# Performance work log

Measured on AMD Instinct MI355X. Metric: run time of the kernel, lower is better.

## Reference

```python
import jax, jax.numpy as jnp
import numpy as np

N_NODES = 50000   # rows of x / output of NF-spmm
M_NODES = 50000   # output of FN-spmm
N_EDGES = 800000
NFEAT, N_HIDDEN, NCLASS = 300, 256, 20
N_IDX = 5000


def setup_inputs() -> dict:
    key = jax.random.key(0)
    ks = jax.random.split(key, 12)
    x = jax.random.normal(ks[0], (N_NODES, NFEAT), dtype=jnp.float32)
    fn_rows = jax.random.randint(ks[1], (N_EDGES,), 0, M_NODES)
    fn_cols = jax.random.randint(ks[2], (N_EDGES,), 0, N_NODES)
    fn_vals = jax.random.uniform(ks[3], (N_EDGES,), dtype=jnp.float32)
    nf_rows = jax.random.randint(ks[4], (N_EDGES,), 0, N_NODES)
    nf_cols = jax.random.randint(ks[5], (N_EDGES,), 0, M_NODES)
    nf_vals = jax.random.uniform(ks[6], (N_EDGES,), dtype=jnp.float32)
    idx = jax.random.randint(ks[7], (N_IDX,), 0, N_NODES)
    # learned parameters (pygcn-style GraphConvolution: spmm(adj, x @ W) + b)
    W1 = jax.random.normal(ks[8], (NFEAT, N_HIDDEN), dtype=jnp.float32) / np.sqrt(NFEAT)
    b1 = jnp.zeros((N_HIDDEN,), dtype=jnp.float32)
    W2 = jax.random.normal(ks[9], (N_HIDDEN, NCLASS), dtype=jnp.float32) / np.sqrt(N_HIDDEN)
    b2 = jnp.zeros((NCLASS,), dtype=jnp.float32)
    return {"x": x, "fn_rows": fn_rows, "fn_cols": fn_cols, "fn_vals": fn_vals,
            "nf_rows": nf_rows, "nf_cols": nf_cols, "nf_vals": nf_vals,
            "idx": idx, "W1": W1, "b1": b1, "W2": W2, "b2": b2}


def _spmm(rows, cols, vals, dense, n_out):
    # sparse(COO) @ dense: gather source rows, scale by edge value, scatter-add.
    return jax.ops.segment_sum(vals[:, None] * dense[cols], rows, num_segments=n_out)


def reference(x, fn_rows, fn_cols, fn_vals, nf_rows, nf_cols, nf_vals, idx, W1, b1, W2, b2):
    # gc1: FN @ (x @ W1) + b1, then relu  (dropout is identity in eval mode)
    h = jax.nn.relu(_spmm(fn_rows, fn_cols, fn_vals, x @ W1, M_NODES) + b1)
    # gc2: NF @ (h @ W2) + b2
    logits = _spmm(nf_rows, nf_cols, nf_vals, h @ W2, N_NODES) + b2
    return jax.nn.softmax(logits, axis=1)[idx]
```

## Files before the change

kernel.cpp:

```cpp
#include <hip/hip_runtime.h>

#define N_NODES 50000
#define M_NODES 50000
#define N_EDGES 800000
#define NFEAT   300
#define NHID    256
#define NCLASS  20
#define N_IDX   5000
#define KTILES  10
#define NTOT    (M_NODES + N_NODES)
#define MARKW   ((N_NODES + 31) / 32)
#define GEMM1_BLOCKS ((N_NODES + 63) / 64)
#define EB4_BLOCKS   ((N_EDGES + 1023) / 1024)

typedef __attribute__((ext_vector_type(8))) short bf16x8;
typedef __attribute__((ext_vector_type(4))) float f32x4;

__device__ inline unsigned short f2bf(float f) {
    unsigned u = __float_as_uint(f);
    u += 0x7fff + ((u >> 16) & 1);
    return (unsigned short)(u >> 16);
}
__device__ inline float bf2f(unsigned short h) { return __uint_as_float((unsigned)h << 16); }
__device__ inline float bflo(unsigned v) { return __uint_as_float(v << 16); }
__device__ inline float bfhi(unsigned v) { return __uint_as_float(v & 0xffff0000u); }

__global__ __launch_bounds__(256) void prep_w1_mark_kernel(const float* __restrict__ W1,
                                                           unsigned short* __restrict__ w1h,
                                                           unsigned short* __restrict__ w1l,
                                                           const int* __restrict__ idx,
                                                           unsigned* __restrict__ markbits) {
    if (blockIdx.x < 320) {
        int id = blockIdx.x * 256 + threadIdx.x;
        int col = id & 255;
        int k   = id >> 8;
        float v = (k < NFEAT) ? W1[(size_t)k * NHID + col] : 0.f;
        unsigned short hi = f2bf(v);
        unsigned short lo = f2bf(v - bf2f(hi));
        size_t off = (size_t)(k >> 5) * (256 * 32) + (size_t)col * 32 + (k & 31);
        w1h[off] = hi;
        w1l[off] = lo;
    } else {
        int i = (blockIdx.x - 320) * 256 + threadIdx.x;
        if (i < N_IDX) {
            int r = idx[i];
            atomicOr(&markbits[r >> 5], 1u << (r & 31));
        }
    }
}

__global__ __launch_bounds__(256) void hist_both_kernel(const int* __restrict__ fn_rows,
                                                        const int* __restrict__ nf_rows,
                                                        const unsigned* __restrict__ markbits,
                                                        int* __restrict__ counts,
                                                        unsigned short* __restrict__ fn_rank,
                                                        unsigned short* __restrict__ nf_rank) {
    const int base = blockIdx.x * 1024 + threadIdx.x;
    int r[4], r2[4], m2[4];
#pragma unroll
    for (int k = 0; k < 4; ++k) {
        int e = base + k * 256;
        r[k]  = (e < N_EDGES) ? fn_rows[e] : -1;
        r2[k] = (e < N_EDGES) ? nf_rows[e] : -1;
    }
#pragma unroll
    for (int k = 0; k < 4; ++k)
        m2[k] = (r2[k] >= 0) ? (int)((markbits[r2[k] >> 5] >> (r2[k] & 31)) & 1u) : 0;
#pragma unroll
    for (int k = 0; k < 4; ++k) {
        if (r[k] >= 0) {
            int p = atomicAdd(&counts[r[k]], 1);
            fn_rank[base + k * 256] = (unsigned short)p;
        }
    }
#pragma unroll
    for (int k = 0; k < 4; ++k) {
        if (m2[k]) {
            int p = atomicAdd(&counts[M_NODES + r2[k]], 1);
            nf_rank[base + k * 256] = (unsigned short)p;
        }
    }
}

__global__ __launch_bounds__(256) void scan_chunk_kernel(const int* __restrict__ counts,
                                                         int* __restrict__ chunk_incl,
                                                         int* __restrict__ chunk_sums, int n) {
    __shared__ int lds[256];
    int i = blockIdx.x * 256 + threadIdx.x;
    int v = (i < n) ? counts[i] : 0;
    lds[threadIdx.x] = v;
    __syncthreads();
    for (int off = 1; off < 256; off <<= 1) {
        int t = (threadIdx.x >= off) ? lds[threadIdx.x - off] : 0;
        __syncthreads();
        lds[threadIdx.x] += t;
        __syncthreads();
    }
    if (i < n) chunk_incl[i] = lds[threadIdx.x];
    if (threadIdx.x == 255) chunk_sums[blockIdx.x] = lds[255];
}

__global__ __launch_bounds__(512) void scan_sums_kernel(const int* __restrict__ chunk_sums,
                                                        int* __restrict__ chunk_off,
                                                        int* __restrict__ row_ptr_end, int nchunks) {
    __shared__ int lds[512];
    int tid = threadIdx.x;
    int v = (tid < nchunks) ? chunk_sums[tid] : 0;
    lds[tid] = v;
    __syncthreads();
    for (int off = 1; off < 512; off <<= 1) {
        int t = (tid >= off) ? lds[tid - off] : 0;
        __syncthreads();
        lds[tid] += t;
        __syncthreads();
    }
    if (tid < nchunks) chunk_off[tid] = lds[tid] - v;
    if (tid == nchunks - 1) *row_ptr_end = lds[tid];
}

__global__ void scan_apply_kernel(const int* __restrict__ counts,
                                  const int* __restrict__ chunk_incl,
                                  const int* __restrict__ chunk_off,
                                  int* __restrict__ row_ptr, int n) {
    int i = blockIdx.x * 256 + threadIdx.x;
    if (i < n) row_ptr[i] = chunk_incl[i] - counts[i] + chunk_off[blockIdx.x];
}

__global__ __launch_bounds__(256) void gemm1_scatter_kernel(
        const float* __restrict__ x,
        const unsigned short* __restrict__ w1h,
        const unsigned short* __restrict__ w1l,
        unsigned short* __restrict__ xwb,
        const int* __restrict__ fn_rows, const int* __restrict__ fn_cols,
        const float* __restrict__ fn_vals,
        const int* __restrict__ nf_rows, const int* __restrict__ nf_cols,
        const float* __restrict__ nf_vals,
        const unsigned* __restrict__ markbits,
        const int* __restrict__ row_ptr,
        const unsigned short* __restrict__ fn_rank,
        const unsigned short* __restrict__ nf_rank,
        uint2* __restrict__ csr_cv) {
    __shared__ unsigned short Ah[2][64 * 40];
    __shared__ unsigned short Al[2][64 * 40];

    if (blockIdx.x >= GEMM1_BLOCKS) {
        const int base = (blockIdx.x - GEMM1_BLOCKS) * 1024 + threadIdx.x;
#pragma unroll
        for (int k = 0; k < 4; ++k) {
            int e = base + k * 256;
            if (e < N_EDGES) {
                int r = fn_rows[e];
                int p = row_ptr[r] + fn_rank[e];
                csr_cv[p] = make_uint2((unsigned)fn_cols[e], __float_as_uint(fn_vals[e]));
            }
        }
#pragma unroll
        for (int k = 0; k < 4; ++k) {
            int e = base + k * 256;
            if (e < N_EDGES) {
                int r2 = nf_rows[e];
                if ((markbits[r2 >> 5] >> (r2 & 31)) & 1u) {
                    int p = row_ptr[M_NODES + r2] + nf_rank[e];
                    csr_cv[p] = make_uint2((unsigned)nf_cols[e], __float_as_uint(nf_vals[e]));
                }
            }
        }
        return;
    }

    const int tid  = threadIdx.x;
    const int lane = tid & 63;
    const int wv   = tid >> 6;
    const int l15  = lane & 15;
    const int g    = lane >> 4;
    const int row0 = blockIdx.x * 64;

    const int sr = tid >> 2;
    const int sc = tid & 3;
    const bool rowok = (row0 + sr) < N_NODES;
    const float* __restrict__ xrow = x + (size_t)(row0 + sr) * NFEAT;

    float cur[8], nxt[8];
    if (rowok) {
        float4 v0 = *(const float4*)&xrow[sc * 8 + 0];
        float4 v1 = *(const float4*)&xrow[sc * 8 + 4];
        cur[0] = v0.x; cur[1] = v0.y; cur[2] = v0.z; cur[3] = v0.w;
        cur[4] = v1.x; cur[5] = v1.y; cur[6] = v1.z; cur[7] = v1.w;
    } else {
#pragma unroll
        for (int j = 0; j < 8; ++j) cur[j] = 0.f;
    }

    f32x4 acc[4][4];
#pragma unroll
    for (int mf = 0; mf < 4; ++mf)
#pragma unroll
        for (int nf = 0; nf < 4; ++nf) acc[mf][nf] = (f32x4){0.f, 0.f, 0.f, 0.f};

    for (int t = 0; t < KTILES; ++t) {
        if (t < KTILES - 1) {
            const int k0 = (t + 1) * 32 + sc * 8;
            if (t + 1 < KTILES - 1) {
                if (rowok) {
                    float4 v0 = *(const float4*)&xrow[k0 + 0];
                    float4 v1 = *(const float4*)&xrow[k0 + 4];
                    nxt[0] = v0.x; nxt[1] = v0.y; nxt[2] = v0.z; nxt[3] = v0.w;
                    nxt[4] = v1.x; nxt[5] = v1.y; nxt[6] = v1.z; nxt[7] = v1.w;
                } else {
#pragma unroll
                    for (int j = 0; j < 8; ++j) nxt[j] = 0.f;
                }
            } else {
#pragma unroll
                for (int j = 0; j < 8; ++j) {
                    int k = k0 + j;
                    nxt[j] = (rowok && k < NFEAT) ? xrow[k] : 0.f;
                }
            }
        }

        {
            bf16x8 hv, lv;
#pragma unroll
            for (int j = 0; j < 8; ++j) {
                unsigned short h = f2bf(cur[j]);
                hv[j] = (short)h;
                lv[j] = (short)f2bf(cur[j] - bf2f(h));
            }
            const int wo = sr * 40 + sc * 8;
            *(bf16x8*)&Ah[t & 1][wo] = hv;
            *(bf16x8*)&Al[t & 1][wo] = lv;
        }
        __syncthreads();

        const int b = t & 1;
        bf16x8 ah[4], al[4];
#pragma unroll
        for (int mf = 0; mf < 4; ++mf) {
            const int ao = (mf * 16 + l15) * 40 + g * 8;
            ah[mf] = *(const bf16x8*)&Ah[b][ao];
            al[mf] = *(const bf16x8*)&Al[b][ao];
        }
        bf16x8 bh[4], bl[4];
#pragma unroll
        for (int nf = 0; nf < 4; ++nf) {
            const size_t bo = (size_t)t * 8192 + (size_t)(wv * 64 + nf * 16 + l15) * 32 + g * 8;
            bh[nf] = *(const bf16x8*)&w1h[bo];
            bl[nf] = *(const bf16x8*)&w1l[bo];
        }
#pragma unroll
        for (int mf = 0; mf < 4; ++mf)
#pragma unroll
            for (int nf = 0; nf < 4; ++nf) {
                acc[mf][nf] = __builtin_amdgcn_mfma_f32_16x16x32_bf16(ah[mf], bh[nf], acc[mf][nf], 0, 0, 0);
                acc[mf][nf] = __builtin_amdgcn_mfma_f32_16x16x32_bf16(ah[mf], bl[nf], acc[mf][nf], 0, 0, 0);
                acc[mf][nf] = __builtin_amdgcn_mfma_f32_16x16x32_bf16(al[mf], bh[nf], acc[mf][nf], 0, 0, 0);
            }
#pragma unroll
        for (int j = 0; j < 8; ++j) cur[j] = nxt[j];
    }

    const int colb = wv * 64;
#pragma unroll
    for (int mf = 0; mf < 4; ++mf) {
        const int rg0 = row0 + mf * 16 + g * 4;
#pragma unroll
        for (int nf = 0; nf < 4; ++nf) {
            const int cg = colb + nf * 16 + l15;
#pragma unroll
            for (int j = 0; j < 4; ++j) {
                const int rg = rg0 + j;
                if (rg < N_NODES) xwb[(size_t)rg * NHID + cg] = f2bf(acc[mf][nf][j]);
            }
        }
    }
}

__global__ __launch_bounds__(128) void spmm_fn_kernel(const int* __restrict__ row_ptr,
                                                      const uint2* __restrict__ csr_cv,
                                                      const unsigned* __restrict__ xwb,
                                                      const float* __restrict__ b1,
                                                      unsigned* __restrict__ hb) {
    const int r = blockIdx.x;
    const int t = threadIdx.x;
    const int s = row_ptr[r], e = row_ptr[r + 1];
    float a0 = 0.f, a1 = 0.f;
    int j = s;
    for (; j + 3 < e; j += 4) {
        uint2 cv0 = csr_cv[j],     cv1 = csr_cv[j + 1];
        uint2 cv2 = csr_cv[j + 2], cv3 = csr_cv[j + 3];
        float v0 = __uint_as_float(cv0.y), v1 = __uint_as_float(cv1.y);
        float v2 = __uint_as_float(cv2.y), v3 = __uint_as_float(cv3.y);
        unsigned x0 = xwb[(size_t)cv0.x * 128 + t];
        unsigned x1 = xwb[(size_t)cv1.x * 128 + t];
        unsigned x2 = xwb[(size_t)cv2.x * 128 + t];
        unsigned x3 = xwb[(size_t)cv3.x * 128 + t];
        a0 += v0 * bflo(x0); a1 += v0 * bfhi(x0);
        a0 += v1 * bflo(x1); a1 += v1 * bfhi(x1);
        a0 += v2 * bflo(x2); a1 += v2 * bfhi(x2);
        a0 += v3 * bflo(x3); a1 += v3 * bfhi(x3);
    }
    for (; j < e; ++j) {
        uint2 cv = csr_cv[j];
        float v = __uint_as_float(cv.y);
        unsigned xv = xwb[(size_t)cv.x * 128 + t];
        a0 += v * bflo(xv); a1 += v * bfhi(xv);
    }
    float2 bv = *(const float2*)&b1[t * 2];
    float o0 = fmaxf(a0 + bv.x, 0.f);
    float o1 = fmaxf(a1 + bv.y, 0.f);
    hb[(size_t)r * 128 + t] = ((unsigned)f2bf(o1) << 16) | (unsigned)f2bf(o0);
}

__global__ __launch_bounds__(256) void gemm2_kernel(const uint4* __restrict__ hb,
                                                    const float* __restrict__ W2,
                                                    float* __restrict__ hw) {
    __shared__ float w2s[NHID * NCLASS];
    for (int i = threadIdx.x; i < NHID * NCLASS; i += 256) w2s[i] = W2[i];
    __syncthreads();
    int gid = blockIdx.x * 256 + threadIdx.x;
    if (gid >= N_NODES * NCLASS) return;
    int row = gid / NCLASS;
    int col = gid - row * NCLASS;
    const uint4* hp = &hb[(size_t)row * 32];
    float acc = 0.f;
#pragma unroll 4
    for (int k8 = 0; k8 < 32; ++k8) {
        uint4 hv = hp[k8];
        int k = k8 * 8;
        acc += bflo(hv.x) * w2s[(k + 0) * NCLASS + col];
        acc += bfhi(hv.x) * w2s[(k + 1) * NCLASS + col];
        acc += bflo(hv.y) * w2s[(k + 2) * NCLASS + col];
        acc += bfhi(hv.y) * w2s[(k + 3) * NCLASS + col];
        acc += bflo(hv.z) * w2s[(k + 4) * NCLASS + col];
        acc += bfhi(hv.z) * w2s[(k + 5) * NCLASS + col];
        acc += bflo(hv.w) * w2s[(k + 6) * NCLASS + col];
        acc += bfhi(hv.w) * w2s[(k + 7) * NCLASS + col];
    }
    hw[gid] = acc;
}

__global__ __launch_bounds__(64) void spmm_nf_softmax_kernel(const int* __restrict__ idx,
                                                             const int* __restrict__ row_ptr,
                                                             const uint2* __restrict__ csr_cv,
                                                             const float* __restrict__ hw,
                                                             const float* __restrict__ b2,
                                                             float* __restrict__ out) {
    const int b    = blockIdx.x;
    const int lane = threadIdx.x;
    const int r = idx[b];
    const int s = row_ptr[M_NODES + r], e = row_ptr[M_NODES + r + 1];

    float acc[NCLASS];
#pragma unroll
    for (int k = 0; k < NCLASS; ++k) acc[k] = 0.f;

    for (int j = s + lane; j < e; j += 64) {
        uint2 cv = csr_cv[j];
        int   c = (int)cv.x;
        float v = __uint_as_float(cv.y);
        const float4* hp = (const float4*)&hw[(size_t)c * NCLASS];
        float4 h0 = hp[0], h1 = hp[1], h2 = hp[2], h3 = hp[3], h4 = hp[4];
        acc[0]  += v * h0.x; acc[1]  += v * h0.y; acc[2]  += v * h0.z; acc[3]  += v * h0.w;
        acc[4]  += v * h1.x; acc[5]  += v * h1.y; acc[6]  += v * h1.z; acc[7]  += v * h1.w;
        acc[8]  += v * h2.x; acc[9]  += v * h2.y; acc[10] += v * h2.z; acc[11] += v * h2.w;
        acc[12] += v * h3.x; acc[13] += v * h3.y; acc[14] += v * h3.z; acc[15] += v * h3.w;
        acc[16] += v * h4.x; acc[17] += v * h4.y; acc[18] += v * h4.z; acc[19] += v * h4.w;
    }

#pragma unroll
    for (int k = 0; k < NCLASS; ++k) {
#pragma unroll
        for (int off = 1; off < 64; off <<= 1) acc[k] += __shfl_xor(acc[k], off, 64);
    }

    if (lane == 0) {
        float v[NCLASS];
        float m = -1e30f;
#pragma unroll
        for (int k = 0; k < NCLASS; ++k) {
            v[k] = acc[k] + b2[k];
            m = fmaxf(m, v[k]);
        }
        float sum = 0.f;
#pragma unroll
        for (int k = 0; k < NCLASS; ++k) {
            v[k] = __expf(v[k] - m);
            sum += v[k];
        }
        float inv = 1.f / sum;
#pragma unroll
        for (int k = 0; k < NCLASS; ++k) out[(size_t)b * NCLASS + k] = v[k] * inv;
    }
}

extern "C" void kernel_launch(void* const* d_in, const int* in_sizes, int n_in,
                              void* d_out, int out_size, void* d_ws, size_t ws_size,
                              hipStream_t stream) {
    const float* x       = (const float*)d_in[0];
    const int*   fn_rows = (const int*)  d_in[1];
    const int*   fn_cols = (const int*)  d_in[2];
    const float* fn_vals = (const float*)d_in[3];
    const int*   nf_rows = (const int*)  d_in[4];
    const int*   nf_cols = (const int*)  d_in[5];
    const float* nf_vals = (const float*)d_in[6];
    const int*   idx     = (const int*)  d_in[7];
    const float* W1      = (const float*)d_in[8];
    const float* b1      = (const float*)d_in[9];
    const float* W2      = (const float*)d_in[10];
    const float* b2      = (const float*)d_in[11];
    float* out = (float*)d_out;

    size_t off = 0;
    auto alloc = [&](size_t bytes) {
        void* p = (char*)d_ws + off;
        off += (bytes + 255) & ~(size_t)255;
        return p;
    };
    unsigned short* xwb = (unsigned short*)alloc((size_t)N_NODES * NHID * 2);
    unsigned*       hb  = (unsigned*)      alloc((size_t)M_NODES * NHID * 2);
    float* hw       = (float*)alloc((size_t)M_NODES * NCLASS * 4);
    int*      counts   = (int*)     alloc((size_t)NTOT * 4);
    unsigned* markbits = (unsigned*)alloc((size_t)MARKW * 4);
    int*   row_ptr  = (int*)  alloc((size_t)(NTOT + 1) * 4);
    uint2* csr_cv   = (uint2*)alloc((size_t)2 * N_EDGES * 8);
    unsigned short* fn_rank = (unsigned short*)alloc((size_t)N_EDGES * 2);
    unsigned short* nf_rank = (unsigned short*)alloc((size_t)N_EDGES * 2);
    int*   chunk_incl = (int*)alloc((size_t)NTOT * 4);
    int*   chunk_sums = (int*)alloc(512 * 4);
    int*   chunk_off  = (int*)alloc(512 * 4);
    unsigned short* w1h = (unsigned short*)alloc((size_t)KTILES * 256 * 32 * 2);
    unsigned short* w1l = (unsigned short*)alloc((size_t)KTILES * 256 * 32 * 2);
    (void)ws_size; (void)n_in; (void)in_sizes; (void)out_size;

    const int NCHUNKS_ALL = (NTOT + 255) / 256;

    size_t zlen = (size_t)((char*)markbits - (char*)counts) + (size_t)MARKW * 4;
    hipMemsetAsync(counts, 0, zlen, stream);

    prep_w1_mark_kernel<<<320 + (N_IDX + 255) / 256, 256, 0, stream>>>(W1, w1h, w1l, idx, markbits);

    hist_both_kernel<<<EB4_BLOCKS, 256, 0, stream>>>(fn_rows, nf_rows, markbits, counts, fn_rank, nf_rank);
    scan_chunk_kernel<<<NCHUNKS_ALL, 256, 0, stream>>>(counts, chunk_incl, chunk_sums, NTOT);
    scan_sums_kernel<<<1, 512, 0, stream>>>(chunk_sums, chunk_off, &row_ptr[NTOT], NCHUNKS_ALL);
    scan_apply_kernel<<<NCHUNKS_ALL, 256, 0, stream>>>(counts, chunk_incl, chunk_off, row_ptr, NTOT);

    gemm1_scatter_kernel<<<GEMM1_BLOCKS + EB4_BLOCKS, 256, 0, stream>>>(
        x, w1h, w1l, xwb,
        fn_rows, fn_cols, fn_vals, nf_rows, nf_cols, nf_vals,
        markbits, row_ptr, fn_rank, nf_rank, csr_cv);

    spmm_fn_kernel<<<M_NODES, 128, 0, stream>>>(row_ptr, csr_cv, (const unsigned*)xwb, b1, hb);

    gemm2_kernel<<<(N_NODES * NCLASS + 255) / 256, 256, 0, stream>>>((const uint4*)hb, W2, hw);

    spmm_nf_softmax_kernel<<<N_IDX, 64, 0, stream>>>(idx, row_ptr, csr_cv, hw, b2, out);
}
```

Before: 201.8 us.

## Use MFMA for second GEMM and merge scan offset kernels

Replaces the scalar LDS-based h@W2 kernel with an MFMA bf16 kernel that uses hi/lo split W2 tiles prepared in the prep kernel, padding NCLASS to 32 columns. It also fuses the single-block chunk-sum scan and the apply kernel into one kernel, where each block reduces its preceding chunk sums itself. This removes a kernel launch and the scalar FMA work in gemm2, at the cost of redundant prefix reductions per block and extra prep work for W2.

```diff
diff --git a/kernel.cpp b/kernel.cpp
--- a/kernel.cpp
+++ b/kernel.cpp
@@ -8,6 +8,7 @@
 #define NCLASS  20
 #define N_IDX   5000
 #define KTILES  10
+#define K2TILES 8
 #define NTOT    (M_NODES + N_NODES)
 #define MARKW   ((N_NODES + 31) / 32)
 #define GEMM1_BLOCKS ((N_NODES + 63) / 64)
@@ -25,11 +26,14 @@
 __device__ inline float bflo(unsigned v) { return __uint_as_float(v << 16); }
 __device__ inline float bfhi(unsigned v) { return __uint_as_float(v & 0xffff0000u); }
 
-__global__ __launch_bounds__(256) void prep_w1_mark_kernel(const float* __restrict__ W1,
-                                                           unsigned short* __restrict__ w1h,
-                                                           unsigned short* __restrict__ w1l,
-                                                           const int* __restrict__ idx,
-                                                           unsigned* __restrict__ markbits) {
+__global__ __launch_bounds__(256) void prep_kernel(const float* __restrict__ W1,
+                                                   unsigned short* __restrict__ w1h,
+                                                   unsigned short* __restrict__ w1l,
+                                                   const int* __restrict__ idx,
+                                                   unsigned* __restrict__ markbits,
+                                                   const float* __restrict__ W2,
+                                                   unsigned short* __restrict__ w2h,
+                                                   unsigned short* __restrict__ w2l) {
     if (blockIdx.x < 320) {
         int id = blockIdx.x * 256 + threadIdx.x;
         int col = id & 255;
@@ -40,12 +44,22 @@
         size_t off = (size_t)(k >> 5) * (256 * 32) + (size_t)col * 32 + (k & 31);
         w1h[off] = hi;
         w1l[off] = lo;
-    } else {
+    } else if (blockIdx.x < 340) {
         int i = (blockIdx.x - 320) * 256 + threadIdx.x;
         if (i < N_IDX) {
             int r = idx[i];
             atomicOr(&markbits[r >> 5], 1u << (r & 31));
         }
+    } else {
+        int id = (blockIdx.x - 340) * 256 + threadIdx.x;
+        int col = id & 31;
+        int k   = id >> 5;
+        float v = (col < NCLASS) ? W2[(size_t)k * NCLASS + col] : 0.f;
+        unsigned short hi = f2bf(v);
+        unsigned short lo = f2bf(v - bf2f(hi));
+        size_t off = (size_t)(k >> 5) * (32 * 32) + (size_t)col * 32 + (k & 31);
+        w2h[off] = hi;
+        w2l[off] = lo;
     }
 }
 
@@ -100,30 +114,25 @@
     if (threadIdx.x == 255) chunk_sums[blockIdx.x] = lds[255];
 }
 
-__global__ __launch_bounds__(512) void scan_sums_kernel(const int* __restrict__ chunk_sums,
-                                                        int* __restrict__ chunk_off,
-                                                        int* __restrict__ row_ptr_end, int nchunks) {
-    __shared__ int lds[512];
-    int tid = threadIdx.x;
-    int v = (tid < nchunks) ? chunk_sums[tid] : 0;
-    lds[tid] = v;
+__global__ __launch_bounds__(256) void scan_finish_kernel(const int* __restrict__ counts,
+                                                          const int* __restrict__ chunk_incl,
+                                                          const int* __restrict__ chunk_sums,
+                                                          int* __restrict__ row_ptr,
+                                                          int n, int nchunks) {
+    __shared__ int lds[256];
+    const int b = blockIdx.x;
+    int partial = 0;
+    for (int i = threadIdx.x; i < b; i += 256) partial += chunk_sums[i];
+    lds[threadIdx.x] = partial;
     __syncthreads();
-    for (int off = 1; off < 512; off <<= 1) {
-        int t = (tid >= off) ? lds[tid - off] : 0;
+    for (int off = 128; off > 0; off >>= 1) {
+        if (threadIdx.x < off) lds[threadIdx.x] += lds[threadIdx.x + off];
         __syncthreads();
-        lds[tid] += t;
-        __syncthreads();
-    }
-    if (tid < nchunks) chunk_off[tid] = lds[tid] - v;
-    if (tid == nchunks - 1) *row_ptr_end = lds[tid];
-}
-
-__global__ void scan_apply_kernel(const int* __restrict__ counts,
-                                  const int* __restrict__ chunk_incl,
-                                  const int* __restrict__ chunk_off,
-                                  int* __restrict__ row_ptr, int n) {
-    int i = blockIdx.x * 256 + threadIdx.x;
-    if (i < n) row_ptr[i] = chunk_incl[i] - counts[i] + chunk_off[blockIdx.x];
+    }
+    const int coff = lds[0];
+    int i = b * 256 + threadIdx.x;
+    if (i < n) row_ptr[i] = chunk_incl[i] - counts[i] + coff;
+    if (b == nchunks - 1 && threadIdx.x == 0) row_ptr[n] = coff + chunk_sums[b];
 }
 
 __global__ __launch_bounds__(256) void gemm1_scatter_kernel(
@@ -312,32 +321,51 @@
     hb[(size_t)r * 128 + t] = ((unsigned)f2bf(o1) << 16) | (unsigned)f2bf(o0);
 }
 
-__global__ __launch_bounds__(256) void gemm2_kernel(const uint4* __restrict__ hb,
-                                                    const float* __restrict__ W2,
-                                                    float* __restrict__ hw) {
-    __shared__ float w2s[NHID * NCLASS];
-    for (int i = threadIdx.x; i < NHID * NCLASS; i += 256) w2s[i] = W2[i];
-    __syncthreads();
-    int gid = blockIdx.x * 256 + threadIdx.x;
-    if (gid >= N_NODES * NCLASS) return;
-    int row = gid / NCLASS;
-    int col = gid - row * NCLASS;
-    const uint4* hp = &hb[(size_t)row * 32];
-    float acc = 0.f;
-#pragma unroll 4
-    for (int k8 = 0; k8 < 32; ++k8) {
-        uint4 hv = hp[k8];
-        int k = k8 * 8;
-        acc += bflo(hv.x) * w2s[(k + 0) * NCLASS + col];
-        acc += bfhi(hv.x) * w2s[(k + 1) * NCLASS + col];
-        acc += bflo(hv.y) * w2s[(k + 2) * NCLASS + col];
-        acc += bfhi(hv.y) * w2s[(k + 3) * NCLASS + col];
-        acc += bflo(hv.z) * w2s[(k + 4) * NCLASS + col];
-        acc += bfhi(hv.z) * w2s[(k + 5) * NCLASS + col];
-        acc += bflo(hv.w) * w2s[(k + 6) * NCLASS + col];
-        acc += bfhi(hv.w) * w2s[(k + 7) * NCLASS + col];
-    }
-    hw[gid] = acc;
+__global__ __launch_bounds__(256) void gemm2_mfma_kernel(const unsigned short* __restrict__ hb,
+                                                         const unsigned short* __restrict__ w2h,
+                                                         const unsigned short* __restrict__ w2l,
+                                                         float* __restrict__ hw) {
+    const int tid  = threadIdx.x;
+    const int lane = tid & 63;
+    const int wv   = tid >> 6;
+    const int l15  = lane & 15;
+    const int g    = lane >> 4;
+    const int row0 = blockIdx.x * 64 + wv * 16;
+    const int arow = row0 + l15;
+    const bool rowok = arow < N_NODES;
+
+    f32x4 acc[2];
+    acc[0] = (f32x4){0.f, 0.f, 0.f, 0.f};
+    acc[1] = (f32x4){0.f, 0.f, 0.f, 0.f};
+
+#pragma unroll
+    for (int t = 0; t < K2TILES; ++t) {
+        bf16x8 a;
+        if (rowok) a = *(const bf16x8*)&hb[(size_t)arow * NHID + t * 32 + g * 8];
+        else {
+#pragma unroll
+            for (int j = 0; j < 8; ++j) a[j] = 0;
+        }
+#pragma unroll
+        for (int nf = 0; nf < 2; ++nf) {
+            const size_t bo = (size_t)t * 1024 + (size_t)(nf * 16 + l15) * 32 + g * 8;
+            bf16x8 bh = *(const bf16x8*)&w2h[bo];
+            bf16x8 bl = *(const bf16x8*)&w2l[bo];
+            acc[nf] = __builtin_amdgcn_mfma_f32_16x16x32_bf16(a, bh, acc[nf], 0, 0, 0);
+            acc[nf] = __builtin_amdgcn_mfma_f32_16x16x32_bf16(a, bl, acc[nf], 0, 0, 0);
+        }
+    }
+
+#pragma unroll
+    for (int nf = 0; nf < 2; ++nf) {
+        const int col = nf * 16 + l15;
+        if (col >= NCLASS) continue;
+#pragma unroll
+        for (int j = 0; j < 4; ++j) {
+            const int row = row0 + g * 4 + j;
+            if (row < N_NODES) hw[(size_t)row * NCLASS + col] = acc[nf][j];
+        }
+    }
 }
 
 __global__ __launch_bounds__(64) void spmm_nf_softmax_kernel(const int* __restrict__ idx,
@@ -428,9 +456,10 @@
     unsigned short* nf_rank = (unsigned short*)alloc((size_t)N_EDGES * 2);
     int*   chunk_incl = (int*)alloc((size_t)NTOT * 4);
     int*   chunk_sums = (int*)alloc(512 * 4);
-    int*   chunk_off  = (int*)alloc(512 * 4);
     unsigned short* w1h = (unsigned short*)alloc((size_t)KTILES * 256 * 32 * 2);
     unsigned short* w1l = (unsigned short*)alloc((size_t)KTILES * 256 * 32 * 2);
+    unsigned short* w2h = (unsigned short*)alloc((size_t)K2TILES * 32 * 32 * 2);
+    unsigned short* w2l = (unsigned short*)alloc((size_t)K2TILES * 32 * 32 * 2);
     (void)ws_size; (void)n_in; (void)in_sizes; (void)out_size;
 
     const int NCHUNKS_ALL = (NTOT + 255) / 256;
@@ -438,12 +467,12 @@
     size_t zlen = (size_t)((char*)markbits - (char*)counts) + (size_t)MARKW * 4;
     hipMemsetAsync(counts, 0, zlen, stream);
 
-    prep_w1_mark_kernel<<<320 + (N_IDX + 255) / 256, 256, 0, stream>>>(W1, w1h, w1l, idx, markbits);
+    prep_kernel<<<372, 256, 0, stream>>>(W1, w1h, w1l, idx, markbits, W2, w2h, w2l);
 
     hist_both_kernel<<<EB4_BLOCKS, 256, 0, stream>>>(fn_rows, nf_rows, markbits, counts, fn_rank, nf_rank);
     scan_chunk_kernel<<<NCHUNKS_ALL, 256, 0, stream>>>(counts, chunk_incl, chunk_sums, NTOT);
-    scan_sums_kernel<<<1, 512, 0, stream>>>(chunk_sums, chunk_off, &row_ptr[NTOT], NCHUNKS_ALL);
-    scan_apply_kernel<<<NCHUNKS_ALL, 256, 0, stream>>>(counts, chunk_incl, chunk_off, row_ptr, NTOT);
+    scan_finish_kernel<<<NCHUNKS_ALL, 256, 0, stream>>>(counts, chunk_incl, chunk_sums,
+                                                        row_ptr, NTOT, NCHUNKS_ALL);
 
     gemm1_scatter_kernel<<<GEMM1_BLOCKS + EB4_BLOCKS, 256, 0, stream>>>(
         x, w1h, w1l, xwb,
@@ -452,7 +481,7 @@
 
     spmm_fn_kernel<<<M_NODES, 128, 0, stream>>>(row_ptr, csr_cv, (const unsigned*)xwb, b1, hb);
 
-    gemm2_kernel<<<(N_NODES * NCLASS + 255) / 256, 256, 0, stream>>>((const uint4*)hb, W2, hw);
+    gemm2_mfma_kernel<<<(N_NODES + 63) / 64, 256, 0, stream>>>((const unsigned short*)hb, w2h, w2l, hw);
 
     spmm_nf_softmax_kernel<<<N_IDX, 64, 0, stream>>>(idx, row_ptr, csr_cv, hw, b2, out);
 }
```

Measured after the change: 189.3 us. 1.07x faster.
